# Optimization experiments

Measured on AMD Instinct MI355X. Metric: run time of the kernel, lower is better.

The kernel has to match this reference:

```python
import jax, jax.numpy as jnp
import numpy as np
from jax import lax


def setup_inputs() -> dict:
    key = jax.random.key(0)
    ks = jax.random.split(key, 6)
    T, B, I, H = 512, 64, 1024, 1024
    f16 = jnp.float16
    # scale weights down so fp16 activations stay in range
    return {
        "x": jax.random.normal(ks[0], (T, B, I), dtype=f16),
        "h0": jax.random.normal(ks[1], (1, B, H), dtype=f16),
        "w_ih": (jax.random.normal(ks[2], (3 * H, I), dtype=f16) * f16(0.02)),
        "w_hh": (jax.random.normal(ks[3], (3 * H, H), dtype=f16) * f16(0.02)),
        "b_ih": jax.random.normal(ks[4], (3 * H,), dtype=f16),
        "b_hh": jax.random.normal(ks[5], (3 * H,), dtype=f16),
    }


def reference(x, h0, w_ih, w_hh, b_ih, b_hh):
    # Single-layer GRU forward, PyTorch gate order (r, z, n).
    # fp16 storage, fp32 accumulation, hidden state re-quantized to fp16
    # each timestep (matches the fused CUDA kernel's shared-memory half buffer).
    f32 = jnp.float32
    H = h0.shape[-1]
    wih = w_ih.astype(f32)   # (3H, I)
    whh = w_hh.astype(f32)   # (3H, H)
    bih = b_ih.astype(f32)
    bhh = b_hh.astype(f32)

    # Precompute input-projection for all timesteps: (T, B, 3H)
    gi = jnp.einsum('tbi,gi->tbg', x.astype(f32), wih) + bih

    def step(h_prev16, gi_t):
        h_prev = h_prev16.astype(f32)                       # (B, H)
        gh = h_prev @ whh.T + bhh                           # (B, 3H)
        ir, iz, inn = gi_t[:, :H], gi_t[:, H:2 * H], gi_t[:, 2 * H:]
        hr, hz, hn = gh[:, :H], gh[:, H:2 * H], gh[:, 2 * H:]
        r = jax.nn.sigmoid(ir + hr)
        z = jax.nn.sigmoid(iz + hz)
        n = jnp.tanh(inn + r * hn)
        h_new = ((1.0 - z) * n + z * h_prev).astype(jnp.float16)
        return h_new, h_new

    _, y = lax.scan(step, h0[0], gi)                        # y: (T, B, H) fp16
    return y
```

## Files before the change

kernel.cpp:

```cpp
#include <hip/hip_runtime.h>
#include <hip/hip_bf16.h>
#include <hip/hip_fp16.h>


typedef __attribute__((ext_vector_type(8))) _Float16 f16x8;
typedef __attribute__((ext_vector_type(4))) float f32x4;
typedef __attribute__((ext_vector_type(8))) float f32x8;

#define MFMA(a, b, c) __builtin_amdgcn_mfma_f32_16x16x32_f16((a), (b), (c), 0, 0, 0)

#define T_T 512
#define T_B 64
#define T_K 1024
#define T_N3 3072

__device__ float          g_gi[(size_t)T_T * T_B * T_N3];
__device__ unsigned short g_hbf[(size_t)T_T * T_B * T_K];
__device__ unsigned       g_flags[64 * 32];

static __device__ __forceinline__ f16x8 cvt8(f32x8 v) {
    f16x8 r;
    #pragma unroll
    for (int i = 0; i < 8; ++i) r[i] = (_Float16)v[i];
    return r;
}
static __device__ __forceinline__ float sigmoidf_(float x) {
    return 1.0f / (1.0f + __expf(-x));
}
static __device__ __forceinline__ float tanhf_(float x) {
    return 2.0f / (1.0f + __expf(-2.0f * x)) - 1.0f;
}

__global__ __launch_bounds__(256) void reset_flags_k() {
    for (int i = threadIdx.x; i < 64 * 32; i += 256) g_flags[i] = 0;
}

__global__ __launch_bounds__(256) void gi_gemm(
    const float* __restrict__ X,
    const float* __restrict__ W,
    const float* __restrict__ bih)
{
    __shared__ unsigned short lA[128 * 32];
    __shared__ unsigned short lB[128 * 32];
    const int tid  = threadIdx.x;
    const int lane = tid & 63;
    const int wid  = tid >> 6;
    const int swz = (blockIdx.x & 7) * 768 + (blockIdx.x >> 3);
    const int m0 = (swz / 24) * 128;
    const int n0 = (swz % 24) * 128;
    const int wm = wid >> 1, wn = wid & 1;

    f32x4 acc[4][4] = {};

    for (int k0 = 0; k0 < T_K; k0 += 32) {
        #pragma unroll
        for (int i = 0; i < 2; ++i) {
            int idx = tid + i * 256;
            int kc  = idx & 3;
            int row = idx >> 2;
            f32x8 va = *(const f32x8*)(X + (size_t)(m0 + row) * T_K + k0 + kc * 8);
            f32x8 vb = *(const f32x8*)(W + (size_t)(n0 + row) * T_K + k0 + kc * 8);
            *(f16x8*)((char*)lA + kc * 2048 + row * 16) = cvt8(va);
            *(f16x8*)((char*)lB + kc * 2048 + row * 16) = cvt8(vb);
        }
        __syncthreads();

        f16x8 a[4], b[4];
        #pragma unroll
        for (int mt = 0; mt < 4; ++mt) {
            int row = 64 * wm + 16 * mt + (lane & 15);
            a[mt] = *(const f16x8*)((const char*)lA + (lane >> 4) * 2048 + row * 16);
        }
        #pragma unroll
        for (int nt = 0; nt < 4; ++nt) {
            int row = 64 * wn + 16 * nt + (lane & 15);
            b[nt] = *(const f16x8*)((const char*)lB + (lane >> 4) * 2048 + row * 16);
        }
        #pragma unroll
        for (int mt = 0; mt < 4; ++mt)
            #pragma unroll
            for (int nt = 0; nt < 4; ++nt)
                acc[mt][nt] = MFMA(a[mt], b[nt], acc[mt][nt]);
        __syncthreads();
    }

    #pragma unroll
    for (int mt = 0; mt < 4; ++mt) {
        int rbase = m0 + 64 * wm + 16 * mt + (lane >> 4) * 4;
        #pragma unroll
        for (int nt = 0; nt < 4; ++nt) {
            int col = n0 + 64 * wn + 16 * nt + (lane & 15);
            float bv = bih[col];
            #pragma unroll
            for (int j = 0; j < 4; ++j)
                g_gi[(size_t)(rbase + j) * T_N3 + col] = acc[mt][nt][j] + bv;
        }
    }
}

__global__ __launch_bounds__(256, 1) void gru_scan(
    const float* __restrict__ Whh,
    const float* __restrict__ Bhh,
    const float* __restrict__ H0,
    float* Y)
{
    __shared__ unsigned short Wl[48 * 1024];
    const int tid  = threadIdx.x;
    const int lane = tid & 63;
    const int w    = tid >> 6;
    const int c0   = blockIdx.x * 16;

    for (int idx = tid; idx < 48 * 128; idx += 256) {
        int row = idx >> 7;
        int kc  = idx & 127;
        int gate = row >> 4, cc = row & 15;
        f32x8 v = *(const f32x8*)(Whh + (size_t)(gate * 1024 + c0 + cc) * T_K + kc * 8);
        *(f16x8*)((char*)Wl + kc * 768 + row * 16) = cvt8(v);
    }
    const int colL = c0 + (lane & 15);
    const float br = Bhh[colL];
    const float bz = Bhh[1024 + colL];
    const float bn = Bhh[2048 + colL];
    __syncthreads();

    const char* bbase = (const char*)Wl + (lane >> 4) * 768 + (lane & 15) * 16;

    float pr[4], pz[4], pn[4];
    #pragma unroll
    for (int j = 0; j < 4; ++j) {
        int row = 16 * w + (lane >> 4) * 4 + j;
        pr[j] = g_gi[(size_t)row * T_N3 + colL];
        pz[j] = g_gi[(size_t)row * T_N3 + 1024 + colL];
        pn[j] = g_gi[(size_t)row * T_N3 + 2048 + colL];
    }

    float hreg[4];

    for (int t = 0; t < T_T; ++t) {
        f32x4 ar = {0.f, 0.f, 0.f, 0.f}, az = ar, an = ar;

        if (t == 0) {
            const float* abase =
                H0 + (size_t)(16 * w + (lane & 15)) * T_K + (lane >> 4) * 8;
            #pragma unroll 4
            for (int kk = 0; kk < 32; ++kk) {
                f16x8 af = cvt8(*(const f32x8*)(abase + kk * 32));
                const char* bb = bbase + kk * 3072;
                ar = MFMA(af, *(const f16x8*)(bb),       ar);
                az = MFMA(af, *(const f16x8*)(bb + 256), az);
                an = MFMA(af, *(const f16x8*)(bb + 512), an);
            }
        } else {
            const unsigned short* abase = g_hbf + (size_t)(t - 1) * (T_B * T_K)
                + (size_t)(16 * w + (lane & 15)) * T_K + (lane >> 4) * 8;
            f16x8 af[32];
            #pragma unroll
            for (int kk = 0; kk < 32; ++kk)
                af[kk] = *(const f16x8*)(abase + kk * 32);
            asm volatile("" ::: "memory");
            #pragma unroll
            for (int kk = 0; kk < 32; ++kk) {
                const char* bb = bbase + kk * 3072;
                ar = MFMA(af[kk], *(const f16x8*)(bb),       ar);
                az = MFMA(af[kk], *(const f16x8*)(bb + 256), az);
                an = MFMA(af[kk], *(const f16x8*)(bb + 512), an);
            }
        }

        #pragma unroll
        for (int j = 0; j < 4; ++j) {
            int row = 16 * w + (lane >> 4) * 4 + j;
            size_t off = (size_t)row * T_K + colL;
            float hp = (t == 0) ? H0[off] : hreg[j];
            float r = sigmoidf_(pr[j] + ar[j] + br);
            float z = sigmoidf_(pz[j] + az[j] + bz);
            float n = tanhf_(pn[j] + r * (an[j] + bn));
            float h = (1.0f - z) * n + z * hp;
            __half h16 = __float2half(h);
            float  hq  = __half2float(h16);
            hreg[j] = hq;
            Y[(size_t)t * (T_B * T_K) + off] = hq;

            unsigned v16 = (unsigned)__half_as_ushort(h16);
            unsigned up  = __shfl_xor(v16, 1);
            if (!(lane & 1)) {
                unsigned packed = v16 | (up << 16);
                unsigned* dst = (unsigned*)(g_hbf + (size_t)t * (T_B * T_K) + off);
                __hip_atomic_store(dst, packed, __ATOMIC_RELAXED,
                                   __HIP_MEMORY_SCOPE_AGENT);
            }
        }

        if (t + 1 < T_T) {
            asm volatile("s_waitcnt vmcnt(0)" ::: "memory");
            __syncthreads();
            if (tid == 0)
                __hip_atomic_store(&g_flags[blockIdx.x * 32], (unsigned)(t + 1),
                                   __ATOMIC_RELAXED, __HIP_MEMORY_SCOPE_AGENT);

            const float* g = g_gi + (size_t)(t + 1) * T_B * T_N3;
            #pragma unroll
            for (int j = 0; j < 4; ++j) {
                int row = 16 * w + (lane >> 4) * 4 + j;
                pr[j] = g[(size_t)row * T_N3 + colL];
                pz[j] = g[(size_t)row * T_N3 + 1024 + colL];
                pn[j] = g[(size_t)row * T_N3 + 2048 + colL];
            }

            if (w == 0) {
                unsigned tgt = (unsigned)(t + 1);
                for (;;) {
                    unsigned v = __hip_atomic_load(&g_flags[lane * 32],
                                                   __ATOMIC_RELAXED,
                                                   __HIP_MEMORY_SCOPE_AGENT);
                    if (__all((int)(v >= tgt))) break;
                    __builtin_amdgcn_s_sleep(1);
                }
            }
            asm volatile("" ::: "memory");
            __syncthreads();
        }
    }
}

extern "C" void kernel_launch(void* const* d_in, const int* in_sizes, int n_in,
                              void* d_out, int out_size, void* d_ws, size_t ws_size,
                              hipStream_t stream)
{
    const float* X   = (const float*)d_in[0];
    const float* H0  = (const float*)d_in[1];
    const float* Wih = (const float*)d_in[2];
    const float* Whh = (const float*)d_in[3];
    const float* Bih = (const float*)d_in[4];
    const float* Bhh = (const float*)d_in[5];
    float* Y = (float*)d_out;
    (void)d_ws; (void)ws_size; (void)in_sizes; (void)n_in; (void)out_size;

    reset_flags_k<<<dim3(1), dim3(256), 0, stream>>>();

    gi_gemm<<<dim3(256 * 24), dim3(256), 0, stream>>>(X, Wih, Bih);

    gru_scan<<<dim3(64), dim3(256), 0, stream>>>(Whh, Bhh, H0, Y);
}
```

Before: 4.404 ms.

## Pre-convert GEMM inputs to fp16 and stage tiles via direct global-to-LDS loads

Adds a conversion kernel that turns the fp32 input sequence and input weights into fp16 buffers once. The input-projection GEMM then loads those fp16 tiles straight into LDS with global_load_lds, using a row-major LDS layout, instead of loading fp32, converting in registers and storing to LDS. This halves GEMM global read traffic and avoids redundant per-tile conversion. The cost is an extra pass over X and W_ih plus a new 64MB scratch buffer, and the new LDS layout may cause bank conflicts on the fragment reads.

```diff
diff --git a/kernel.cpp b/kernel.cpp
--- a/kernel.cpp
+++ b/kernel.cpp
@@ -17,6 +17,8 @@
 __device__ float          g_gi[(size_t)T_T * T_B * T_N3];
 __device__ unsigned short g_hbf[(size_t)T_T * T_B * T_K];
 __device__ unsigned       g_flags[64 * 32];
+__device__ unsigned short g_xh[(size_t)T_T * T_B * T_K];
+__device__ unsigned short g_wh[(size_t)T_N3 * T_K];
 
 static __device__ __forceinline__ f16x8 cvt8(f32x8 v) {
     f16x8 r;
@@ -35,13 +37,25 @@
     for (int i = threadIdx.x; i < 64 * 32; i += 256) g_flags[i] = 0;
 }
 
+__global__ __launch_bounds__(256) void cvt_k(
+    const float* __restrict__ X,
+    const float* __restrict__ W)
+{
+    const size_t NX = (size_t)T_T * T_B * T_K / 8;
+    const size_t NW = (size_t)T_N3 * T_K / 8;
+    size_t i0 = (size_t)blockIdx.x * 256 + threadIdx.x;
+    size_t stride = (size_t)gridDim.x * 256;
+    for (size_t i = i0; i < NX; i += stride)
+        ((f16x8*)g_xh)[i] = cvt8(((const f32x8*)X)[i]);
+    for (size_t i = i0; i < NW; i += stride)
+        ((f16x8*)g_wh)[i] = cvt8(((const f32x8*)W)[i]);
+}
+
 __global__ __launch_bounds__(256) void gi_gemm(
-    const float* __restrict__ X,
-    const float* __restrict__ W,
     const float* __restrict__ bih)
 {
-    __shared__ unsigned short lA[128 * 32];
-    __shared__ unsigned short lB[128 * 32];
+    __shared__ __align__(16) unsigned short lA[128 * 32];
+    __shared__ __align__(16) unsigned short lB[128 * 32];
     const int tid  = threadIdx.x;
     const int lane = tid & 63;
     const int wid  = tid >> 6;
@@ -50,18 +64,26 @@
     const int n0 = (swz % 24) * 128;
     const int wm = wid >> 1, wn = wid & 1;
 
+    const int srow = tid >> 2;
+    const int skc  = tid & 3;
+
     f32x4 acc[4][4] = {};
 
     for (int k0 = 0; k0 < T_K; k0 += 32) {
         #pragma unroll
         for (int i = 0; i < 2; ++i) {
-            int idx = tid + i * 256;
-            int kc  = idx & 3;
-            int row = idx >> 2;
-            f32x8 va = *(const f32x8*)(X + (size_t)(m0 + row) * T_K + k0 + kc * 8);
-            f32x8 vb = *(const f32x8*)(W + (size_t)(n0 + row) * T_K + k0 + kc * 8);
-            *(f16x8*)((char*)lA + kc * 2048 + row * 16) = cvt8(va);
-            *(f16x8*)((char*)lB + kc * 2048 + row * 16) = cvt8(vb);
+            const unsigned short* ga =
+                g_xh + (size_t)(m0 + i * 64 + srow) * T_K + k0 + skc * 8;
+            const unsigned short* gb =
+                g_wh + (size_t)(n0 + i * 64 + srow) * T_K + k0 + skc * 8;
+            char* la = (char*)lA + i * 4096 + wid * 1024;
+            char* lb = (char*)lB + i * 4096 + wid * 1024;
+            __builtin_amdgcn_global_load_lds(
+                (const __attribute__((address_space(1))) unsigned int*)ga,
+                (__attribute__((address_space(3))) unsigned int*)la, 16, 0, 0);
+            __builtin_amdgcn_global_load_lds(
+                (const __attribute__((address_space(1))) unsigned int*)gb,
+                (__attribute__((address_space(3))) unsigned int*)lb, 16, 0, 0);
         }
         __syncthreads();
 
@@ -69,12 +91,12 @@
         #pragma unroll
         for (int mt = 0; mt < 4; ++mt) {
             int row = 64 * wm + 16 * mt + (lane & 15);
-            a[mt] = *(const f16x8*)((const char*)lA + (lane >> 4) * 2048 + row * 16);
+            a[mt] = *(const f16x8*)((const char*)lA + row * 64 + (lane >> 4) * 16);
         }
         #pragma unroll
         for (int nt = 0; nt < 4; ++nt) {
             int row = 64 * wn + 16 * nt + (lane & 15);
-            b[nt] = *(const f16x8*)((const char*)lB + (lane >> 4) * 2048 + row * 16);
+            b[nt] = *(const f16x8*)((const char*)lB + row * 64 + (lane >> 4) * 16);
         }
         #pragma unroll
         for (int mt = 0; mt < 4; ++mt)
@@ -238,7 +260,9 @@
 
     reset_flags_k<<<dim3(1), dim3(256), 0, stream>>>();
 
-    gi_gemm<<<dim3(256 * 24), dim3(256), 0, stream>>>(X, Wih, Bih);
+    cvt_k<<<dim3(2048), dim3(256), 0, stream>>>(X, Wih);
+
+    gi_gemm<<<dim3(256 * 24), dim3(256), 0, stream>>>(Bih);
 
     gru_scan<<<dim3(64), dim3(256), 0, stream>>>(Whh, Bhh, H0, Y);
 }
```

Result: no change. 4.366 ms (-0.9%).

## Fuse input-projection GEMM with GRU scan to overlap them via progress counters

Applied to the files above, without the earlier changes.

Merges the input-projection GEMM and the recurrent scan into one launch. The first 64 blocks run the scan, and the remaining blocks compute GEMM tiles, bumping per-row-tile completion counters. Scan blocks wait only until the gi rows for the next timestep are ready, so the long GEMM can overlap the serial recurrence instead of running entirely before it. This relies on scan blocks being scheduled first and staying co-resident. The GEMM blocks now also occupy the full 96KB of shared memory and run at occupancy 1, which may slow the GEMM itself.

```diff
diff --git a/kernel.cpp b/kernel.cpp
--- a/kernel.cpp
+++ b/kernel.cpp
@@ -13,10 +13,14 @@
 #define T_B 64
 #define T_K 1024
 #define T_N3 3072
+#define N_SCAN 64
+#define N_GEMM 6144
 
 __device__ float          g_gi[(size_t)T_T * T_B * T_N3];
 __device__ unsigned short g_hbf[(size_t)T_T * T_B * T_K];
 __device__ unsigned       g_flags[64 * 32];
+__device__ unsigned       g_mtc[256 * 32];
+__device__ unsigned       g_gdone[32];
 
 static __device__ __forceinline__ f16x8 cvt8(f32x8 v) {
     f16x8 r;
@@ -33,82 +37,96 @@
 
 __global__ __launch_bounds__(256) void reset_flags_k() {
     for (int i = threadIdx.x; i < 64 * 32; i += 256) g_flags[i] = 0;
-}
-
-__global__ __launch_bounds__(256) void gi_gemm(
+    for (int i = threadIdx.x; i < 256 * 32; i += 256) g_mtc[i] = 0;
+    if (threadIdx.x < 32) g_gdone[threadIdx.x] = 0;
+}
+
+__global__ __launch_bounds__(256, 1) void fused_k(
     const float* __restrict__ X,
-    const float* __restrict__ W,
-    const float* __restrict__ bih)
-{
-    __shared__ unsigned short lA[128 * 32];
-    __shared__ unsigned short lB[128 * 32];
-    const int tid  = threadIdx.x;
-    const int lane = tid & 63;
-    const int wid  = tid >> 6;
-    const int swz = (blockIdx.x & 7) * 768 + (blockIdx.x >> 3);
-    const int m0 = (swz / 24) * 128;
-    const int n0 = (swz % 24) * 128;
-    const int wm = wid >> 1, wn = wid & 1;
-
-    f32x4 acc[4][4] = {};
-
-    for (int k0 = 0; k0 < T_K; k0 += 32) {
-        #pragma unroll
-        for (int i = 0; i < 2; ++i) {
-            int idx = tid + i * 256;
-            int kc  = idx & 3;
-            int row = idx >> 2;
-            f32x8 va = *(const f32x8*)(X + (size_t)(m0 + row) * T_K + k0 + kc * 8);
-            f32x8 vb = *(const f32x8*)(W + (size_t)(n0 + row) * T_K + k0 + kc * 8);
-            *(f16x8*)((char*)lA + kc * 2048 + row * 16) = cvt8(va);
-            *(f16x8*)((char*)lB + kc * 2048 + row * 16) = cvt8(vb);
-        }
-        __syncthreads();
-
-        f16x8 a[4], b[4];
-        #pragma unroll
-        for (int mt = 0; mt < 4; ++mt) {
-            int row = 64 * wm + 16 * mt + (lane & 15);
-            a[mt] = *(const f16x8*)((const char*)lA + (lane >> 4) * 2048 + row * 16);
-        }
-        #pragma unroll
-        for (int nt = 0; nt < 4; ++nt) {
-            int row = 64 * wn + 16 * nt + (lane & 15);
-            b[nt] = *(const f16x8*)((const char*)lB + (lane >> 4) * 2048 + row * 16);
-        }
-        #pragma unroll
-        for (int mt = 0; mt < 4; ++mt)
-            #pragma unroll
-            for (int nt = 0; nt < 4; ++nt)
-                acc[mt][nt] = MFMA(a[mt], b[nt], acc[mt][nt]);
-        __syncthreads();
-    }
-
-    #pragma unroll
-    for (int mt = 0; mt < 4; ++mt) {
-        int rbase = m0 + 64 * wm + 16 * mt + (lane >> 4) * 4;
-        #pragma unroll
-        for (int nt = 0; nt < 4; ++nt) {
-            int col = n0 + 64 * wn + 16 * nt + (lane & 15);
-            float bv = bih[col];
-            #pragma unroll
-            for (int j = 0; j < 4; ++j)
-                g_gi[(size_t)(rbase + j) * T_N3 + col] = acc[mt][nt][j] + bv;
-        }
-    }
-}
-
-__global__ __launch_bounds__(256, 1) void gru_scan(
+    const float* __restrict__ Wih,
     const float* __restrict__ Whh,
+    const float* __restrict__ Bih,
     const float* __restrict__ Bhh,
     const float* __restrict__ H0,
     float* Y)
 {
-    __shared__ unsigned short Wl[48 * 1024];
-    const int tid  = threadIdx.x;
+    __shared__ __align__(16) unsigned short smem[48 * 1024];
+    const int tid = threadIdx.x;
+    const int bid = blockIdx.x;
+
+    if (bid >= N_SCAN) {
+        const int g    = bid - N_SCAN;
+        const int lane = tid & 63;
+        const int wid  = tid >> 6;
+        const int m0 = (g / 24) * 128;
+        const int n0 = (g % 24) * 128;
+        const int wm = wid >> 1, wn = wid & 1;
+        unsigned short* lA = smem;
+        unsigned short* lB = smem + 4096;
+
+        f32x4 acc[4][4] = {};
+
+        for (int k0 = 0; k0 < T_K; k0 += 32) {
+            #pragma unroll
+            for (int i = 0; i < 2; ++i) {
+                int idx = tid + i * 256;
+                int kc  = idx & 3;
+                int row = idx >> 2;
+                f32x8 va = *(const f32x8*)(X + (size_t)(m0 + row) * T_K + k0 + kc * 8);
+                f32x8 vb = *(const f32x8*)(Wih + (size_t)(n0 + row) * T_K + k0 + kc * 8);
+                *(f16x8*)((char*)lA + kc * 2048 + row * 16) = cvt8(va);
+                *(f16x8*)((char*)lB + kc * 2048 + row * 16) = cvt8(vb);
+            }
+            __syncthreads();
+
+            f16x8 a[4], b[4];
+            #pragma unroll
+            for (int mt = 0; mt < 4; ++mt) {
+                int row = 64 * wm + 16 * mt + (lane & 15);
+                a[mt] = *(const f16x8*)((const char*)lA + (lane >> 4) * 2048 + row * 16);
+            }
+            #pragma unroll
+            for (int nt = 0; nt < 4; ++nt) {
+                int row = 64 * wn + 16 * nt + (lane & 15);
+                b[nt] = *(const f16x8*)((const char*)lB + (lane >> 4) * 2048 + row * 16);
+            }
+            #pragma unroll
+            for (int mt = 0; mt < 4; ++mt)
+                #pragma unroll
+                for (int nt = 0; nt < 4; ++nt)
+                    acc[mt][nt] = MFMA(a[mt], b[nt], acc[mt][nt]);
+            __syncthreads();
+        }
+
+        #pragma unroll
+        for (int mt = 0; mt < 4; ++mt) {
+            int rbase = m0 + 64 * wm + 16 * mt + (lane >> 4) * 4;
+            #pragma unroll
+            for (int nt = 0; nt < 4; ++nt) {
+                int col = n0 + 64 * wn + 16 * nt + (lane & 15);
+                float bv = Bih[col];
+                #pragma unroll
+                for (int j = 0; j < 4; ++j)
+                    __hip_atomic_store(&g_gi[(size_t)(rbase + j) * T_N3 + col],
+                                       acc[mt][nt][j] + bv,
+                                       __ATOMIC_RELAXED, __HIP_MEMORY_SCOPE_AGENT);
+            }
+        }
+        asm volatile("s_waitcnt vmcnt(0)" ::: "memory");
+        __syncthreads();
+        if (tid == 0) {
+            __hip_atomic_fetch_add(&g_mtc[(g / 24) * 32], 1u,
+                                   __ATOMIC_RELAXED, __HIP_MEMORY_SCOPE_AGENT);
+            __hip_atomic_fetch_add(&g_gdone[0], 1u,
+                                   __ATOMIC_RELAXED, __HIP_MEMORY_SCOPE_AGENT);
+        }
+        return;
+    }
+
+    unsigned short* Wl = smem;
     const int lane = tid & 63;
     const int w    = tid >> 6;
-    const int c0   = blockIdx.x * 16;
+    const int c0   = bid * 16;
 
     for (int idx = tid; idx < 48 * 128; idx += 256) {
         int row = idx >> 7;
@@ -124,6 +142,22 @@
     __syncthreads();
 
     const char* bbase = (const char*)Wl + (lane >> 4) * 768 + (lane & 15) * 16;
+
+    bool all_done = false;
+    int  gmax = -1;
+
+    {
+        for (;;) {
+            unsigned gd = __hip_atomic_load(&g_gdone[0], __ATOMIC_RELAXED,
+                                            __HIP_MEMORY_SCOPE_AGENT);
+            if (gd >= (unsigned)N_GEMM) { all_done = true; break; }
+            unsigned v = __hip_atomic_load(&g_mtc[0], __ATOMIC_RELAXED,
+                                           __HIP_MEMORY_SCOPE_AGENT);
+            if (v >= 24u) break;
+            __builtin_amdgcn_s_sleep(8);
+        }
+        gmax = 0;
+    }
 
     float pr[4], pz[4], pn[4];
     #pragma unroll
@@ -195,8 +229,26 @@
             asm volatile("s_waitcnt vmcnt(0)" ::: "memory");
             __syncthreads();
             if (tid == 0)
-                __hip_atomic_store(&g_flags[blockIdx.x * 32], (unsigned)(t + 1),
+                __hip_atomic_store(&g_flags[bid * 32], (unsigned)(t + 1),
                                    __ATOMIC_RELAXED, __HIP_MEMORY_SCOPE_AGENT);
+
+            if (!all_done) {
+                int needed = (t + 1) >> 1;
+                if (needed > gmax) {
+                    for (;;) {
+                        unsigned gd = __hip_atomic_load(&g_gdone[0],
+                                                        __ATOMIC_RELAXED,
+                                                        __HIP_MEMORY_SCOPE_AGENT);
+                        if (gd >= (unsigned)N_GEMM) { all_done = true; break; }
+                        unsigned v = __hip_atomic_load(&g_mtc[needed * 32],
+                                                       __ATOMIC_RELAXED,
+                                                       __HIP_MEMORY_SCOPE_AGENT);
+                        if (v >= 24u) break;
+                        __builtin_amdgcn_s_sleep(8);
+                    }
+                    gmax = needed;
+                }
+            }
 
             const float* g = g_gi + (size_t)(t + 1) * T_B * T_N3;
             #pragma unroll
@@ -238,7 +290,6 @@
 
     reset_flags_k<<<dim3(1), dim3(256), 0, stream>>>();
 
-    gi_gemm<<<dim3(256 * 24), dim3(256), 0, stream>>>(X, Wih, Bih);
-
-    gru_scan<<<dim3(64), dim3(256), 0, stream>>>(Whh, Bhh, H0, Y);
-}
+    fused_k<<<dim3(N_SCAN + N_GEMM), dim3(256), 0, stream>>>(
+        X, Wih, Whh, Bih, Bhh, H0, Y);
+}
```

Result: faster. 4.056 ms (-7.9%).
